# Optimization experiments

Measured on AMD Instinct MI355X. Metric: run time of the kernel, lower is better.

Reference implementation:

```python
import jax, jax.numpy as jnp
import numpy as np

B, CIN, COUT, T, H, W, NH = 8, 16, 16, 32, 16, 16, 4
DIN = CIN * H * W    # 4096
DOUT = COUT * H * W  # 4096
DH = DOUT // NH      # 1024


def conv3d(x, w, b, pad):
    y = jax.lax.conv_general_dilated(
        x, w, window_strides=(1, 1, 1), padding=((pad, pad),) * 3,
        dimension_numbers=('NCDHW', 'OIDHW', 'NCDHW'))
    return y + b[None, :, None, None, None]


def instance_norm(x, eps=1e-5):
    # InstanceNorm3d default: no affine, normalize per (B,C) over (T,H,W)
    mu = x.mean(axis=(2, 3, 4), keepdims=True)
    var = ((x - mu) ** 2).mean(axis=(2, 3, 4), keepdims=True)
    return (x - mu) * jax.lax.rsqrt(var + eps)


def slstm(x, Wg, bg, Rg):
    # x: (B,T,D). Wg: (4,D,D) input weights [i,f,z,o]; bg: (4,D);
    # Rg: (NH,4,DH,DH) block-diagonal per-head recurrent weights.
    Bb, Tt, D = x.shape
    Gx = jnp.einsum('btd,god->btgo', x, Wg) + bg  # (B,T,4,D)

    def step(carry, gx):
        h, c, n, m = carry
        hh = h.reshape(Bb, NH, DH)
        gh = jnp.einsum('bhd,hgod->bhgo', hh, Rg)          # (B,NH,4,DH)
        pre = gx + gh.transpose(0, 2, 1, 3).reshape(Bb, 4, D)
        i_pre, f_pre, z_pre, o_pre = pre[:, 0], pre[:, 1], pre[:, 2], pre[:, 3]
        # stabilized exponential gating (xLSTM sLSTM)
        m_new = jnp.maximum(f_pre + m, i_pre)
        i = jnp.exp(i_pre - m_new)
        f = jnp.exp(f_pre + m - m_new)
        c = f * c + i * jnp.tanh(z_pre)
        n = f * n + i
        h = jax.nn.sigmoid(o_pre) * c / n
        return (h, c, n, m_new), h

    init = tuple(jnp.zeros((Bb, D), x.dtype) for _ in range(4))
    _, hs = jax.lax.scan(step, init, Gx.transpose(1, 0, 2, 3))  # hs: (T,B,D)
    return hs.transpose(1, 0, 2)


def setup_inputs():
    key = jax.random.key(0)
    ks = jax.random.split(key, 8)
    s = 0.02
    return {
        'x': jax.random.normal(ks[0], (B, CIN, T, H, W), jnp.float32),
        'c1_w': jax.random.normal(ks[1], (COUT, CIN, 3, 3, 3), jnp.float32) * 0.05,
        'c1_b': jnp.zeros((COUT,), jnp.float32),
        'c2_w': jax.random.normal(ks[2], (COUT, COUT, 3, 3, 3), jnp.float32) * 0.05,
        'c2_b': jnp.zeros((COUT,), jnp.float32),
        'c3_w': jax.random.normal(ks[3], (COUT, COUT, 3, 3, 3), jnp.float32) * 0.05,
        'c3_b': jnp.zeros((COUT,), jnp.float32),
        'pre_w': jax.random.normal(ks[4], (DOUT, DIN), jnp.float32) * s,
        'pre_b': jnp.zeros((DOUT,), jnp.float32),
        'lstm_W': jax.random.normal(ks[5], (4, DOUT, DOUT), jnp.float32) * s,
        'lstm_b': jnp.zeros((4, DOUT), jnp.float32),
        'lstm_R': jax.random.normal(ks[6], (NH, 4, DH, DH), jnp.float32) * s,
        'attn_w': jax.random.normal(ks[7], (1, 2 * COUT), jnp.float32) * 0.05,
        'attn_b': jnp.zeros((1,), jnp.float32),
    }


def reference(x, c1_w, c1_b, c2_w, c2_b, c3_w, c3_b, pre_w, pre_b,
              lstm_W, lstm_b, lstm_R, attn_w, attn_b):
    # conv3d branch: conv -> IN -> relu -> conv -> relu -> conv -> relu
    y = jax.nn.relu(instance_norm(conv3d(x, c1_w, c1_b, 1)))
    y = jax.nn.relu(conv3d(y, c2_w, c2_b, 1))
    out3d = jax.nn.relu(conv3d(y, c3_w, c3_b, 1))
    # sLSTM branch
    xs = x.transpose(0, 2, 1, 3, 4).reshape(B, T, DIN)
    xs = xs @ pre_w.T + pre_b
    hs = slstm(xs, lstm_W, lstm_b, lstm_R)                 # (B,T,DOUT)
    s_out = hs.reshape(B, T, COUT, H, W).transpose(0, 2, 1, 3, 4)
    # attention-gated fusion: cat -> 1x1x1 conv -> sigmoid -> weighted sum
    comb = jnp.concatenate([s_out, out3d], axis=1)         # (B,2*COUT,T,H,W)
    alpha = jax.nn.sigmoid(jnp.einsum('bcthw,oc->bothw', comb, attn_w)
                           + attn_b[None, :, None, None, None])
    return alpha * out3d + (1 - alpha) * s_out
```

## Files before the change

kernel.cpp:

```cpp
#include <hip/hip_runtime.h>
#include <hip/hip_bf16.h>
#include <cstddef>

#define BB   8
#define CIN  16
#define COUT 16
#define TT   32
#define HH   16
#define WW   16
#define DIN  4096
#define DOUT 4096
#define NH   4
#define DH   1024
#define SPAT 8192
#define NSEQ 256

typedef __attribute__((ext_vector_type(8))) short  bf16x8;
typedef __attribute__((ext_vector_type(4))) float  f32x4;
typedef __attribute__((ext_vector_type(4))) unsigned short us4;
typedef __attribute__((ext_vector_type(4))) int    i32x4;
typedef unsigned short ushort_t;
typedef unsigned long long u64_t;

static __device__ __forceinline__ ushort_t f2bf(float f) {
    union { float f; unsigned u; } v; v.f = f;
    unsigned r = (v.u + 0x7fffu + ((v.u >> 16) & 1u)) >> 16;
    return (ushort_t)r;
}
static __device__ __forceinline__ float bf2f(ushort_t u) {
    union { unsigned u; float f; } v; v.u = ((unsigned)u) << 16;
    return v.f;
}

__global__ void setup_kernel(const float* __restrict__ x, ushort_t* __restrict__ xt,
                             const float* __restrict__ w1, const float* __restrict__ w2,
                             const float* __restrict__ w3,
                             float* __restrict__ cw1, float* __restrict__ cw2,
                             float* __restrict__ cw3, int* __restrict__ flags) {
    int bid = blockIdx.x;
    if (bid < 1024) {
        int idx = bid * 256 + threadIdx.x;
        int n = idx >> 10, k4 = (idx & 1023) * 4;
        int b = n >> 5, t = n & 31, c = k4 >> 8, hw = k4 & 255;
        f32x4 f = *(const f32x4*)&x[(((size_t)(b * CIN + c) * TT + t)) * 256 + hw];
        us4 o;
        #pragma unroll
        for (int i = 0; i < 4; ++i) o[i] = f2bf(f[i]);
        *(us4*)&xt[(size_t)n * DIN + k4] = o;
    } else if (bid < 1105) {
        int i = (bid - 1024) * 256 + threadIdx.x;
        if (i < 3 * 6912) {
            int set = i / 6912, j = i - set * 6912;
            const float* w = (set == 0) ? w1 : (set == 1) ? w2 : w3;
            float* cw      = (set == 0) ? cw1 : (set == 1) ? cw2 : cw3;
            int o = j & 15, r = j >> 4;
            int k = r % 27, ci = r / 27;
            cw[j] = w[(size_t)(o * CIN + ci) * 27 + k];
        }
    } else {
        int j = (bid - 1105) * 256 + threadIdx.x;
        if (j < 2176)
            ((i32x4*)flags)[j] = (i32x4){0, 0, 0, 0};
    }
}

template<int BN, int BK, bool OUT_BF16, bool ADD_BIAS>
__device__ __forceinline__
void gemm_body(char* smem, int bx, int by, int nsplit,
               const ushort_t* __restrict__ A, const float* __restrict__ B,
               const float* __restrict__ bias, void* __restrict__ C,
               int N, int K) {
    constexpr int NF  = BN / 16;
    constexpr int TPR = 256 / BN;
    constexpr int FPT = BK / TPR;
    ushort_t* Al = (ushort_t*)smem;
    ushort_t* Bl = Al + 2 * 256 * BK;
    int tid  = threadIdx.x;
    int lane = tid & 63;
    int wv   = tid >> 6;
    int n0 = bx * BN;
    int ksp = K / nsplit;
    int kS  = by * ksp;

    f32x4 acc[4][NF];
    #pragma unroll
    for (int i = 0; i < 4; ++i)
        #pragma unroll
        for (int j = 0; j < NF; ++j) acc[i][j] = (f32x4){0.f, 0.f, 0.f, 0.f};

    auto stageA = [&](int buf, int k0) {
        #pragma unroll
        for (int q = 0; q < 8; ++q) {
            int rbase = wv * 64 + q * 8;
            int row = rbase + (lane >> 3);
            const ushort_t* g = A + (size_t)row * K + k0 + (lane & 7) * 8;
            __builtin_amdgcn_global_load_lds(
                (const __attribute__((address_space(1))) void*)g,
                (__attribute__((address_space(3))) void*)&Al[(buf * 256 + rbase) * BK],
                16, 0, 0);
        }
    };
    auto stageB = [&](int buf, int k0) {
        int r  = tid / TPR;
        int cs = (tid % TPR) * FPT;
        const float* g = B + (size_t)(n0 + r) * K + k0 + cs;
        #pragma unroll
        for (int q = 0; q < FPT / 4; ++q) {
            f32x4 f = *(const f32x4*)(g + q * 4);
            us4 pk;
            #pragma unroll
            for (int e = 0; e < 4; ++e) pk[e] = f2bf(f[e]);
            *(us4*)&Bl[(buf * BN + r) * BK + cs + q * 4] = pk;
        }
    };
    auto compute = [&](int buf) {
        #pragma unroll
        for (int ks = 0; ks < BK / 32; ++ks) {
            bf16x8 af[4], bfr[NF];
            #pragma unroll
            for (int i = 0; i < 4; ++i)
                af[i] = *(const bf16x8*)&Al[(buf * 256 + wv * 64 + i * 16 + (lane & 15)) * BK + ks * 32 + (lane >> 4) * 8];
            #pragma unroll
            for (int j = 0; j < NF; ++j)
                bfr[j] = *(const bf16x8*)&Bl[(buf * BN + j * 16 + (lane & 15)) * BK + ks * 32 + (lane >> 4) * 8];
            #pragma unroll
            for (int i = 0; i < 4; ++i)
                #pragma unroll
                for (int j = 0; j < NF; ++j)
                    acc[i][j] = __builtin_amdgcn_mfma_f32_16x16x32_bf16(af[i], bfr[j], acc[i][j], 0, 0, 0);
        }
    };

    stageA(0, kS); stageB(0, kS);
    __syncthreads();
    int nk = ksp / BK;
    int cur = 0;
    for (int t = 0; t < nk; ++t) {
        if (t + 1 < nk) { stageA(cur ^ 1, kS + (t + 1) * BK); stageB(cur ^ 1, kS + (t + 1) * BK); }
        compute(cur);
        __syncthreads();
        cur ^= 1;
    }

    size_t cofs = (size_t)by * 256 * N;
    #pragma unroll
    for (int i = 0; i < 4; ++i) {
        int row = wv * 64 + i * 16 + (lane >> 4) * 4;
        #pragma unroll
        for (int j = 0; j < NF; ++j) {
            int col = n0 + j * 16 + (lane & 15);
            float bv = ADD_BIAS ? bias[col] : 0.f;
            #pragma unroll
            for (int r = 0; r < 4; ++r) {
                float v = acc[i][j][r] + bv;
                if constexpr (OUT_BF16) ((ushort_t*)C)[cofs + (size_t)(row + r) * N + col] = f2bf(v);
                else                    ((float*)C)[cofs + (size_t)(row + r) * N + col] = v;
            }
        }
    }
}

__device__ __forceinline__
void conv_taps(const float* xin, const float* __restrict__ cw, int half,
               const float* __restrict__ bias, float* accs, int tid) {
    int h = tid >> 4, wx = tid & 15;
    f32x4 a0 = *(const f32x4*)&bias[half * 8];
    f32x4 a1 = *(const f32x4*)&bias[half * 8 + 4];
    for (int ci = 0; ci < CIN; ++ci) {
        #pragma unroll
        for (int kt = 0; kt < 3; ++kt) {
            #pragma unroll
            for (int kh = 0; kh < 3; ++kh) {
                int h2 = h + kh - 1;
                bool vh = (unsigned)h2 < HH;
                int h2c = vh ? h2 : 0;
                #pragma unroll
                for (int kw = 0; kw < 3; ++kw) {
                    int w2 = wx + kw - 1;
                    bool v = vh && ((unsigned)w2 < WW);
                    int w2c = ((unsigned)w2 < WW) ? w2 : 0;
                    float xv = xin[(ci * 3 + kt) * 256 + h2c * 16 + w2c];
                    xv = v ? xv : 0.f;
                    const float* wp = cw + (size_t)(ci * 27 + kt * 9 + kh * 3 + kw) * 16 + half * 8;
                    f32x4 w0 = *(const f32x4*)(wp);
                    f32x4 w1 = *(const f32x4*)(wp + 4);
                    a0 += xv * w0; a1 += xv * w1;
                }
            }
        }
    }
    #pragma unroll
    for (int i = 0; i < 4; ++i) { accs[i] = a0[i]; accs[4 + i] = a1[i]; }
}

__device__ __forceinline__
void conv1_body(char* smem, int blk,
                const float* __restrict__ in, const float* __restrict__ cw,
                const float* __restrict__ bias,
                float* __restrict__ out, float* __restrict__ psum) {
    float* xin = (float*)smem;
    int b = blk >> 6, t = (blk >> 1) & 31, half = blk & 1;
    int tid = threadIdx.x;

    for (int i = tid; i < CIN * 3 * 256; i += 256) {
        int hw = i & 255, r = i >> 8;
        int kt = r % 3, ci = r / 3;
        int tt = t + kt - 1;
        float v = 0.f;
        if ((unsigned)tt < TT)
            v = in[((size_t)(b * CIN + ci) * TT + tt) * 256 + hw];
        xin[(ci * 3 + kt) * 256 + hw] = v;
    }
    __syncthreads();

    float accs[8];
    conv_taps(xin, cw, half, bias, accs, tid);
    #pragma unroll
    for (int o = 0; o < 8; ++o)
        out[((size_t)(b * COUT + half * 8 + o) * TT + t) * 256 + tid] = accs[o];

    __syncthreads();
    float* sm = xin;
    int wv = tid >> 6;
    #pragma unroll
    for (int o = 0; o < 8; ++o) {
        float s = accs[o];
        float q = accs[o] * accs[o];
        #pragma unroll
        for (int m = 1; m < 64; m <<= 1) {
            s += __shfl_xor(s, m, 64);
            q += __shfl_xor(q, m, 64);
        }
        if ((tid & 63) == 0) { sm[wv * 16 + o * 2] = s; sm[wv * 16 + o * 2 + 1] = q; }
    }
    __syncthreads();
    if (tid < 16) {
        int o = tid >> 1, which = tid & 1;
        float v = sm[o * 2 + which] + sm[16 + o * 2 + which]
                + sm[32 + o * 2 + which] + sm[48 + o * 2 + which];
        psum[((((size_t)(b * 32 + t) * 2 + half) * 8 + o) * 2) + which] = v;
    }
}

__device__ __forceinline__
void conv2_body(char* smem, int blk,
                const float* __restrict__ y1, const float* __restrict__ cw,
                const float* __restrict__ bias, const float* __restrict__ psum,
                float* __restrict__ y2, int* __restrict__ cflags) {
    float* xin = (float*)smem;
    float* sstats = xin + 12288;
    int b = blk >> 6, t = (blk >> 1) & 31, half = blk & 1;
    int tid = threadIdx.x;

    if (tid < 16) {
        int c = tid;
        float sum = 0.f, sq = 0.f;
        for (int t2 = 0; t2 < 32; ++t2) {
            size_t base = (((size_t)(b * 32 + t2) * 2 + (c >> 3)) * 8 + (c & 7)) * 2;
            sum += psum[base];
            sq  += psum[base + 1];
        }
        float mu = sum / (float)SPAT;
        float var = sq / (float)SPAT - mu * mu;
        sstats[c * 2]     = mu;
        sstats[c * 2 + 1] = rsqrtf(var + 1e-5f);
    }
    __syncthreads();

    for (int i = tid; i < CIN * 3 * 256; i += 256) {
        int hw = i & 255, r = i >> 8;
        int kt = r % 3, ci = r / 3;
        int tt = t + kt - 1;
        float v = 0.f;
        if ((unsigned)tt < TT) {
            v = y1[((size_t)(b * CIN + ci) * TT + tt) * 256 + hw];
            v = fmaxf((v - sstats[ci * 2]) * sstats[ci * 2 + 1], 0.f);
        }
        xin[(ci * 3 + kt) * 256 + hw] = v;
    }
    __syncthreads();

    float accs[8];
    conv_taps(xin, cw, half, bias, accs, tid);
    #pragma unroll
    for (int o = 0; o < 8; ++o) {
        float v = fmaxf(accs[o], 0.f);
        __hip_atomic_store(&y2[((size_t)(b * COUT + half * 8 + o) * TT + t) * 256 + tid],
                           v, __ATOMIC_RELAXED, __HIP_MEMORY_SCOPE_AGENT);
    }
    __syncthreads();
    if (tid == 0)
        __hip_atomic_store(&cflags[blk], 1, __ATOMIC_RELAXED, __HIP_MEMORY_SCOPE_AGENT);
}

__device__ __forceinline__
void conv3_body(char* smem, int blk,
                const float* __restrict__ y2, const float* __restrict__ cw,
                const float* __restrict__ bias, float* __restrict__ out3d,
                const int* __restrict__ cflags) {
    float* xin = (float*)smem;
    int b = blk >> 6, t = (blk >> 1) & 31, half = blk & 1;
    int tid = threadIdx.x;

    if (tid == 0) {
        #pragma unroll
        for (int dt = -1; dt <= 1; ++dt) {
            int tn = t + dt;
            if ((unsigned)tn >= TT) continue;
            #pragma unroll
            for (int hh = 0; hh < 2; ++hh) {
                const int* f = &cflags[(b << 6) | (tn << 1) | hh];
                while (__hip_atomic_load(f, __ATOMIC_RELAXED,
                                         __HIP_MEMORY_SCOPE_AGENT) == 0)
                    __builtin_amdgcn_s_sleep(1);
            }
        }
    }
    __syncthreads();

    for (int i = tid; i < CIN * 3 * 256; i += 256) {
        int hw = i & 255, r = i >> 8;
        int kt = r % 3, ci = r / 3;
        int tt = t + kt - 1;
        float v = 0.f;
        if ((unsigned)tt < TT)
            v = __hip_atomic_load(&y2[((size_t)(b * CIN + ci) * TT + tt) * 256 + hw],
                                  __ATOMIC_RELAXED, __HIP_MEMORY_SCOPE_AGENT);
        xin[(ci * 3 + kt) * 256 + hw] = v;
    }
    __syncthreads();

    float accs[8];
    conv_taps(xin, cw, half, bias, accs, tid);
    #pragma unroll
    for (int o = 0; o < 8; ++o)
        out3d[((size_t)(b * COUT + half * 8 + o) * TT + t) * 256 + tid] = fmaxf(accs[o], 0.f);
}

__global__ __launch_bounds__(256, 2)
void fused1_kernel(const ushort_t* __restrict__ xt, const float* __restrict__ pre_w,
                   const float* __restrict__ pre_b, ushort_t* __restrict__ xs2b,
                   const float* __restrict__ x, const float* __restrict__ cw1,
                   const float* __restrict__ c1_b, float* __restrict__ y1,
                   float* __restrict__ psum) {
    extern __shared__ char smem[];
    if (blockIdx.x < 256)
        gemm_body<16, 64, true, true>(smem, blockIdx.x, 0, 1, xt, pre_w, pre_b, xs2b, DOUT, DIN);
    else
        conv1_body(smem, blockIdx.x - 256, x, cw1, c1_b, y1, psum);
}

__global__ __launch_bounds__(256, 2)
void fused2_kernel(const ushort_t* __restrict__ xs2b, const float* __restrict__ lstm_W,
                   float* __restrict__ Gx,
                   const float* __restrict__ y1, const float* __restrict__ cw2,
                   const float* __restrict__ c2_b, const float* __restrict__ psum,
                   float* __restrict__ y2,
                   const float* __restrict__ cw3, const float* __restrict__ c3_b,
                   float* __restrict__ out3d, int* __restrict__ cflags) {
    extern __shared__ char smem[];
    if (blockIdx.x < 1024)
        gemm_body<32, 64, false, false>(smem, blockIdx.x & 511, blockIdx.x >> 9, 2,
                                        xs2b, lstm_W, nullptr, Gx, 4 * DOUT, DOUT);
    else if (blockIdx.x < 1536)
        conv2_body(smem, blockIdx.x - 1024, y1, cw2, c2_b, psum, y2, cflags);
    else
        conv3_body(smem, blockIdx.x - 1536, y2, cw3, c3_b, out3d, cflags);
}

#define GXPS ((size_t)NSEQ * 4 * DOUT)

__global__ __launch_bounds__(256, 1)
void lstm_persist_kernel(const float* __restrict__ R,
                         const float* __restrict__ Gx,
                         const float* __restrict__ lstm_b,
                         unsigned* __restrict__ hfr,
                         int* __restrict__ flags,
                         const float* __restrict__ out3d,
                         const float* __restrict__ attn_w,
                         const float* __restrict__ attn_b,
                         float* __restrict__ out) {
    __shared__ ushort_t Rl[4][32][64 * 8];
    __shared__ float gh_p[4][4][16][8];

    int tid  = threadIdx.x;
    int lane = tid & 63;
    int w    = tid >> 6;
    int head = blockIdx.x >> 6;
    int oc   = blockIdx.x & 63;

    #pragma unroll 4
    for (int n = 0; n < 64; ++n) {
        int g = n >> 4, r = n & 15;
        const float* src = R + ((size_t)((head * 4 + g) * DH + oc * 16 + r)) * DH + tid * 4;
        f32x4 f = *(const f32x4*)src;
        int k0 = tid * 4;
        int ks = k0 >> 5;
        int kI = (k0 >> 3) & 3;
        int e8 = k0 & 7;
        union { ushort_t u[4]; u64_t q; } pk;
        #pragma unroll
        for (int e = 0; e < 4; ++e) pk.u[e] = f2bf(f[e]);
        *(u64_t*)&Rl[g][ks][((kI << 4) | r) * 8 + e8] = pk.q;
    }

    int arow = lane & 15;
    int part = arow >> 3;
    int bb   = arow & 7;
    int kseg = lane >> 4;

    int gb  = tid >> 4;
    int gol = tid & 15;
    int gd  = head * DH + oc * 16 + gol;
    int o_h = oc * 16 + gol;
    unsigned hslot = ((unsigned)head * 32 + (o_h >> 5)) * 256 + gb * 32 + (o_h & 31);
    float c_r = 0.f, n_r = 0.f, m_r = 0.f;
    float lb0 = 0.f, lb1 = 0.f, lb2 = 0.f, lb3 = 0.f;
    if (tid < 128) {
        lb0 = lstm_b[gd];
        lb1 = lstm_b[DOUT + gd];
        lb2 = lstm_b[2 * DOUT + gd];
        lb3 = lstm_b[3 * DOUT + gd];
    }

    __syncthreads();

    for (int t = 0; t < TT; ++t) {
        float gx0 = lb0, gx1 = lb1, gx2 = lb2, gx3 = lb3;
        if (tid < 128) {
            size_t gxoff = ((size_t)(gb * TT + t)) * (4 * DOUT) + gd;
            #pragma unroll
            for (int p = 0; p < 2; ++p) {
                const float* gp = Gx + p * GXPS + gxoff;
                gx0 += gp[0];
                gx1 += gp[DOUT];
                gx2 += gp[2 * DOUT];
                gx3 += gp[3 * DOUT];
            }
        }

        if (t > 0) {
            const int* fl = flags + (((t - 1) * 4 + head) << 6);
            for (;;) {
                int v = __hip_atomic_load(fl + lane, __ATOMIC_RELAXED,
                                          __HIP_MEMORY_SCOPE_AGENT);
                if (__all(v != 0)) break;
                __builtin_amdgcn_s_sleep(1);
            }

            const u64_t* hb = (const u64_t*)hfr
                + ((((size_t)(t - 1) * 4 + head) * 32) * 256 + bb * 32 + kseg * 8) / 2;
            bf16x8 hf[8];
            #pragma unroll
            for (int j = 0; j < 8; ++j) {
                const u64_t* p = hb + (size_t)(w * 8 + j) * 128;
                union { ushort_t u[8]; bf16x8 v; } fr;
                #pragma unroll
                for (int e2 = 0; e2 < 4; ++e2) {
                    u64_t q = __hip_atomic_load(p + e2, __ATOMIC_RELAXED,
                                                __HIP_MEMORY_SCOPE_AGENT);
                    unsigned q0 = (unsigned)q, q1 = (unsigned)(q >> 32);
                    fr.u[e2 * 2]     = part ? (ushort_t)(q0 >> 16) : (ushort_t)(q0 & 0xffffu);
                    fr.u[e2 * 2 + 1] = part ? (ushort_t)(q1 >> 16) : (ushort_t)(q1 & 0xffffu);
                }
                hf[j] = fr.v;
            }

            f32x4 acc[4];
            #pragma unroll
            for (int g = 0; g < 4; ++g) acc[g] = (f32x4){0.f, 0.f, 0.f, 0.f};
            #pragma unroll
            for (int g = 0; g < 4; ++g)
                #pragma unroll
                for (int j = 0; j < 8; ++j) {
                    bf16x8 a = *(const bf16x8*)&Rl[g][w * 8 + j][lane * 8];
                    acc[g] = __builtin_amdgcn_mfma_f32_16x16x32_bf16(a, hf[j], acc[g], 0, 0, 0);
                }
            #pragma unroll
            for (int g = 0; g < 4; ++g)
                #pragma unroll
                for (int r = 0; r < 4; ++r)
                    acc[g][r] += __shfl_xor(acc[g][r], 8, 64);
            if (part == 0) {
                int orow0 = kseg * 4;
                #pragma unroll
                for (int g = 0; g < 4; ++g)
                    #pragma unroll
                    for (int r = 0; r < 4; ++r)
                        gh_p[w][g][orow0 + r][bb] = acc[g][r];
            }
        } else {
            for (int i = tid; i < 4 * 4 * 16 * 8; i += 256)
                ((float*)gh_p)[i] = 0.f;
        }
        __syncthreads();

        if (tid < 128) {
            float ip = gx0 +
                gh_p[0][0][gol][gb] + gh_p[1][0][gol][gb] + gh_p[2][0][gol][gb] + gh_p[3][0][gol][gb];
            float fp = gx1 +
                gh_p[0][1][gol][gb] + gh_p[1][1][gol][gb] + gh_p[2][1][gol][gb] + gh_p[3][1][gol][gb];
            float zp = gx2 +
                gh_p[0][2][gol][gb] + gh_p[1][2][gol][gb] + gh_p[2][2][gol][gb] + gh_p[3][2][gol][gb];
            float op = gx3 +
                gh_p[0][3][gol][gb] + gh_p[1][3][gol][gb] + gh_p[2][3][gol][gb] + gh_p[3][3][gol][gb];
            float mn = fmaxf(fp + m_r, ip);
            float iv = __expf(ip - mn);
            float fv = __expf(fp + m_r - mn);
            float zc = fminf(fmaxf(zp, -9.f), 9.f);
            float th = 1.f - 2.f / (__expf(2.f * zc) + 1.f);
            c_r = fv * c_r + iv * th;
            n_r = fv * n_r + iv;
            float sig = 1.f / (1.f + __expf(-op));
            float hv = sig * c_r / n_r;
            m_r = mn;
            unsigned hi = f2bf(hv);
            unsigned lo = f2bf(hv - bf2f((ushort_t)hi));
            __hip_atomic_store(&hfr[(size_t)t * 32768 + hslot],
                               hi | (lo << 16),
                               __ATOMIC_RELAXED, __HIP_MEMORY_SCOPE_AGENT);
        }
        __syncthreads();
        if (tid == 0)
            __hip_atomic_store(&flags[((t * 4 + head) << 6) + oc], 1,
                               __ATOMIC_RELAXED, __HIP_MEMORY_SCOPE_AGENT);
    }

    {
        const int* fl31 = flags + ((31 * 4) << 6);
        for (;;) {
            int ok = 1;
            #pragma unroll
            for (int q = 0; q < 4; ++q)
                ok &= (__hip_atomic_load(fl31 + q * 64 + lane, __ATOMIC_RELAXED,
                                         __HIP_MEMORY_SCOPE_AGENT) != 0);
            if (__all(ok)) break;
            __builtin_amdgcn_s_sleep(1);
        }

        int idx = blockIdx.x * 256 + tid;
        int hw = idx & 255;
        int tC = (idx >> 8) & 31;
        int bC = idx >> 13;
        float dot = attn_b[0];
        float sv[16], ov[16];
        #pragma unroll
        for (int ch = 0; ch < 16; ++ch) {
            int d = ch * 256 + hw;
            int hd2 = d >> 10, o_h2 = d & 1023;
            size_t slot = (size_t)tC * 32768 + (size_t)hd2 * 8192
                        + (o_h2 >> 5) * 256 + bC * 32 + (o_h2 & 31);
            unsigned v32 = __hip_atomic_load(&hfr[slot], __ATOMIC_RELAXED,
                                             __HIP_MEMORY_SCOPE_AGENT);
            float s = bf2f((ushort_t)(v32 & 0xffffu)) + bf2f((ushort_t)(v32 >> 16));
            float o3 = out3d[(((size_t)(bC * COUT + ch) * TT + tC)) * 256 + hw];
            sv[ch] = s; ov[ch] = o3;
            dot += attn_w[ch] * s + attn_w[16 + ch] * o3;
        }
        float alpha = 1.f / (1.f + expf(-dot));
        #pragma unroll
        for (int ch = 0; ch < 16; ++ch) {
            out[(((size_t)(bC * COUT + ch) * TT + tC)) * 256 + hw] =
                alpha * ov[ch] + (1.f - alpha) * sv[ch];
        }
    }
}

extern "C" void kernel_launch(void* const* d_in, const int* in_sizes, int n_in,
                              void* d_out, int out_size, void* d_ws, size_t ws_size,
                              hipStream_t stream) {
    const float* x      = (const float*)d_in[0];
    const float* c1_w   = (const float*)d_in[1];
    const float* c1_b   = (const float*)d_in[2];
    const float* c2_w   = (const float*)d_in[3];
    const float* c2_b   = (const float*)d_in[4];
    const float* c3_w   = (const float*)d_in[5];
    const float* c3_b   = (const float*)d_in[6];
    const float* pre_w  = (const float*)d_in[7];
    const float* pre_b  = (const float*)d_in[8];
    const float* lstm_W = (const float*)d_in[9];
    const float* lstm_b = (const float*)d_in[10];
    const float* lstm_R = (const float*)d_in[11];
    const float* attn_w = (const float*)d_in[12];
    const float* attn_b = (const float*)d_in[13];
    float* out = (float*)d_out;

    float* wsf = (float*)d_ws;
    float* y1    = wsf;
    float* y2    = y1 + 1048576;
    float* out3d = y2 + 1048576;
    float* Gx    = out3d + 1048576;
    float* cw1   = Gx + 2 * 4194304;
    float* cw2   = cw1 + 6912;
    float* cw3   = cw2 + 6912;
    float* psum  = cw3 + 6912;
    float* pad   = psum + 8192;
    ushort_t* xt   = (ushort_t*)(pad + 64);
    ushort_t* xs2b = xt + 1048576;
    unsigned* hfr  = (unsigned*)(xs2b + 1048576);
    int*     flags = (int*)(hfr + 1048576);
    int*    cflags = flags + 8192;

    setup_kernel<<<1114, 256, 0, stream>>>(x, xt, c1_w, c2_w, c3_w, cw1, cw2, cw3, flags);

    fused1_kernel<<<768, 256, 69632, stream>>>(xt, pre_w, pre_b, xs2b,
                                               x, cw1, c1_b, y1, psum);

    fused2_kernel<<<2048, 256, 73728, stream>>>(xs2b, lstm_W, Gx,
                                                y1, cw2, c2_b, psum, y2,
                                                cw3, c3_b, out3d, cflags);

    lstm_persist_kernel<<<256, 256, 0, stream>>>(lstm_R, Gx, lstm_b, hfr, flags,
                                                 out3d, attn_w, attn_b, out);
}
```

Baseline: 528.6 us.

## Move input-gate GEMM into persistent LSTM kernel prologue, drop split-K

Moves the Gx = xs @ W GEMM out of the fused conv kernel and into a prologue of the persistent sLSTM kernel. Each of the 256 blocks computes the gate preactivations for exactly the 16 columns per gate that it consumes in the recurrence, adds the bias, and writes them to a block-private buffer. This removes the split-K partial sums, the double Gx read in the recurrence, and the contention between GEMM and conv work in fused2. The cost is that the GEMM now runs on only 256 blocks at one block per CU, serialized before the recurrence, and the conv kernel no longer overlaps with it.

```diff
diff --git a/kernel.cpp b/kernel.cpp
--- a/kernel.cpp
+++ b/kernel.cpp
@@ -66,7 +66,7 @@
 
 template<int BN, int BK, bool OUT_BF16, bool ADD_BIAS>
 __device__ __forceinline__
-void gemm_body(char* smem, int bx, int by, int nsplit,
+void gemm_body(char* smem, int bx,
                const ushort_t* __restrict__ A, const float* __restrict__ B,
                const float* __restrict__ bias, void* __restrict__ C,
                int N, int K) {
@@ -79,8 +79,6 @@
     int lane = tid & 63;
     int wv   = tid >> 6;
     int n0 = bx * BN;
-    int ksp = K / nsplit;
-    int kS  = by * ksp;
 
     f32x4 acc[4][NF];
     #pragma unroll
@@ -131,18 +129,17 @@
         }
     };
 
-    stageA(0, kS); stageB(0, kS);
-    __syncthreads();
-    int nk = ksp / BK;
+    stageA(0, 0); stageB(0, 0);
+    __syncthreads();
+    int nk = K / BK;
     int cur = 0;
     for (int t = 0; t < nk; ++t) {
-        if (t + 1 < nk) { stageA(cur ^ 1, kS + (t + 1) * BK); stageB(cur ^ 1, kS + (t + 1) * BK); }
+        if (t + 1 < nk) { stageA(cur ^ 1, (t + 1) * BK); stageB(cur ^ 1, (t + 1) * BK); }
         compute(cur);
         __syncthreads();
         cur ^= 1;
     }
 
-    size_t cofs = (size_t)by * 256 * N;
     #pragma unroll
     for (int i = 0; i < 4; ++i) {
         int row = wv * 64 + i * 16 + (lane >> 4) * 4;
@@ -153,8 +150,8 @@
             #pragma unroll
             for (int r = 0; r < 4; ++r) {
                 float v = acc[i][j][r] + bv;
-                if constexpr (OUT_BF16) ((ushort_t*)C)[cofs + (size_t)(row + r) * N + col] = f2bf(v);
-                else                    ((float*)C)[cofs + (size_t)(row + r) * N + col] = v;
+                if constexpr (OUT_BF16) ((ushort_t*)C)[(size_t)(row + r) * N + col] = f2bf(v);
+                else                    ((float*)C)[(size_t)(row + r) * N + col] = v;
             }
         }
     }
@@ -345,50 +342,127 @@
                    float* __restrict__ psum) {
     extern __shared__ char smem[];
     if (blockIdx.x < 256)
-        gemm_body<16, 64, true, true>(smem, blockIdx.x, 0, 1, xt, pre_w, pre_b, xs2b, DOUT, DIN);
+        gemm_body<16, 64, true, true>(smem, blockIdx.x, xt, pre_w, pre_b, xs2b, DOUT, DIN);
     else
         conv1_body(smem, blockIdx.x - 256, x, cw1, c1_b, y1, psum);
 }
 
 __global__ __launch_bounds__(256, 2)
-void fused2_kernel(const ushort_t* __restrict__ xs2b, const float* __restrict__ lstm_W,
-                   float* __restrict__ Gx,
-                   const float* __restrict__ y1, const float* __restrict__ cw2,
+void fused2_kernel(const float* __restrict__ y1, const float* __restrict__ cw2,
                    const float* __restrict__ c2_b, const float* __restrict__ psum,
                    float* __restrict__ y2,
                    const float* __restrict__ cw3, const float* __restrict__ c3_b,
                    float* __restrict__ out3d, int* __restrict__ cflags) {
     extern __shared__ char smem[];
-    if (blockIdx.x < 1024)
-        gemm_body<32, 64, false, false>(smem, blockIdx.x & 511, blockIdx.x >> 9, 2,
-                                        xs2b, lstm_W, nullptr, Gx, 4 * DOUT, DOUT);
-    else if (blockIdx.x < 1536)
-        conv2_body(smem, blockIdx.x - 1024, y1, cw2, c2_b, psum, y2, cflags);
+    if (blockIdx.x < 512)
+        conv2_body(smem, blockIdx.x, y1, cw2, c2_b, psum, y2, cflags);
     else
-        conv3_body(smem, blockIdx.x - 1536, y2, cw3, c3_b, out3d, cflags);
-}
-
-#define GXPS ((size_t)NSEQ * 4 * DOUT)
+        conv3_body(smem, blockIdx.x - 512, y2, cw3, c3_b, out3d, cflags);
+}
 
 __global__ __launch_bounds__(256, 1)
 void lstm_persist_kernel(const float* __restrict__ R,
-                         const float* __restrict__ Gx,
+                         const ushort_t* __restrict__ xs2b,
+                         const float* __restrict__ lstm_W,
                          const float* __restrict__ lstm_b,
+                         float* __restrict__ Gxp,
                          unsigned* __restrict__ hfr,
                          int* __restrict__ flags,
                          const float* __restrict__ out3d,
                          const float* __restrict__ attn_w,
                          const float* __restrict__ attn_b,
                          float* __restrict__ out) {
-    __shared__ ushort_t Rl[4][32][64 * 8];
-    __shared__ float gh_p[4][4][16][8];
+    __shared__ char smem[139264];
 
     int tid  = threadIdx.x;
     int lane = tid & 63;
     int w    = tid >> 6;
     int head = blockIdx.x >> 6;
     int oc   = blockIdx.x & 63;
-
+    int gcbase = head * DH + oc * 16;
+
+    {
+        ushort_t* Al = (ushort_t*)smem;
+        ushort_t* Bl = Al + 2 * 256 * 64;
+        f32x4 acc[4][4];
+        #pragma unroll
+        for (int i = 0; i < 4; ++i)
+            #pragma unroll
+            for (int j = 0; j < 4; ++j) acc[i][j] = (f32x4){0.f, 0.f, 0.f, 0.f};
+
+        auto stageA = [&](int buf, int k0) {
+            #pragma unroll
+            for (int q = 0; q < 8; ++q) {
+                int rbase = w * 64 + q * 8;
+                int row = rbase + (lane >> 3);
+                const ushort_t* g = xs2b + (size_t)row * DIN + k0 + (lane & 7) * 8;
+                __builtin_amdgcn_global_load_lds(
+                    (const __attribute__((address_space(1))) void*)g,
+                    (__attribute__((address_space(3))) void*)&Al[(buf * 256 + rbase) * 64],
+                    16, 0, 0);
+            }
+        };
+        auto stageB = [&](int buf, int k0) {
+            int r = tid >> 2;
+            int g = r >> 4, ol = r & 15;
+            size_t gc = (size_t)g * DOUT + gcbase + ol;
+            int cs = (tid & 3) * 16;
+            const float* p = lstm_W + gc * DOUT + k0 + cs;
+            #pragma unroll
+            for (int q = 0; q < 4; ++q) {
+                f32x4 f = *(const f32x4*)(p + q * 4);
+                us4 pk;
+                #pragma unroll
+                for (int e = 0; e < 4; ++e) pk[e] = f2bf(f[e]);
+                *(us4*)&Bl[(buf * 64 + r) * 64 + cs + q * 4] = pk;
+            }
+        };
+        auto compute = [&](int buf) {
+            #pragma unroll
+            for (int ks = 0; ks < 2; ++ks) {
+                bf16x8 af[4], bfr[4];
+                #pragma unroll
+                for (int i = 0; i < 4; ++i)
+                    af[i] = *(const bf16x8*)&Al[(buf * 256 + w * 64 + i * 16 + (lane & 15)) * 64 + ks * 32 + (lane >> 4) * 8];
+                #pragma unroll
+                for (int j = 0; j < 4; ++j)
+                    bfr[j] = *(const bf16x8*)&Bl[(buf * 64 + j * 16 + (lane & 15)) * 64 + ks * 32 + (lane >> 4) * 8];
+                #pragma unroll
+                for (int i = 0; i < 4; ++i)
+                    #pragma unroll
+                    for (int j = 0; j < 4; ++j)
+                        acc[i][j] = __builtin_amdgcn_mfma_f32_16x16x32_bf16(af[i], bfr[j], acc[i][j], 0, 0, 0);
+            }
+        };
+
+        stageA(0, 0); stageB(0, 0);
+        __syncthreads();
+        int cur = 0;
+        for (int t = 0; t < 64; ++t) {
+            if (t + 1 < 64) { stageA(cur ^ 1, (t + 1) * 64); stageB(cur ^ 1, (t + 1) * 64); }
+            compute(cur);
+            __syncthreads();
+            cur ^= 1;
+        }
+
+        float* myGx = Gxp + (size_t)blockIdx.x * 16384;
+        #pragma unroll
+        for (int i = 0; i < 4; ++i) {
+            int row = w * 64 + i * 16 + (lane >> 4) * 4;
+            #pragma unroll
+            for (int j = 0; j < 4; ++j) {
+                int ol = lane & 15;
+                float bv = lstm_b[(size_t)j * DOUT + gcbase + ol];
+                #pragma unroll
+                for (int r = 0; r < 4; ++r)
+                    myGx[((j * 256 + row + r) << 4) + ol] = acc[i][j][r] + bv;
+            }
+        }
+    }
+    __syncthreads();
+
+    ushort_t* Rl = (ushort_t*)smem;
+    float* gh_p  = (float*)(smem + 131072);
     #pragma unroll 4
     for (int n = 0; n < 64; ++n) {
         int g = n >> 4, r = n & 15;
@@ -401,7 +475,7 @@
         union { ushort_t u[4]; u64_t q; } pk;
         #pragma unroll
         for (int e = 0; e < 4; ++e) pk.u[e] = f2bf(f[e]);
-        *(u64_t*)&Rl[g][ks][((kI << 4) | r) * 8 + e8] = pk.q;
+        *(u64_t*)&Rl[((g * 32 + ks) << 9) + ((kI << 4) | r) * 8 + e8] = pk.q;
     }
 
     int arow = lane & 15;
@@ -411,32 +485,21 @@
 
     int gb  = tid >> 4;
     int gol = tid & 15;
-    int gd  = head * DH + oc * 16 + gol;
     int o_h = oc * 16 + gol;
     unsigned hslot = ((unsigned)head * 32 + (o_h >> 5)) * 256 + gb * 32 + (o_h & 31);
     float c_r = 0.f, n_r = 0.f, m_r = 0.f;
-    float lb0 = 0.f, lb1 = 0.f, lb2 = 0.f, lb3 = 0.f;
-    if (tid < 128) {
-        lb0 = lstm_b[gd];
-        lb1 = lstm_b[DOUT + gd];
-        lb2 = lstm_b[2 * DOUT + gd];
-        lb3 = lstm_b[3 * DOUT + gd];
-    }
+    const float* myGx = Gxp + (size_t)blockIdx.x * 16384;
 
     __syncthreads();
 
     for (int t = 0; t < TT; ++t) {
-        float gx0 = lb0, gx1 = lb1, gx2 = lb2, gx3 = lb3;
+        float gx0 = 0.f, gx1 = 0.f, gx2 = 0.f, gx3 = 0.f;
         if (tid < 128) {
-            size_t gxoff = ((size_t)(gb * TT + t)) * (4 * DOUT) + gd;
-            #pragma unroll
-            for (int p = 0; p < 2; ++p) {
-                const float* gp = Gx + p * GXPS + gxoff;
-                gx0 += gp[0];
-                gx1 += gp[DOUT];
-                gx2 += gp[2 * DOUT];
-                gx3 += gp[3 * DOUT];
-            }
+            const float* gp = myGx + (((gb * 32 + t)) << 4) + gol;
+            gx0 = gp[0];
+            gx1 = gp[1 * 4096];
+            gx2 = gp[2 * 4096];
+            gx3 = gp[3 * 4096];
         }
 
         if (t > 0) {
@@ -473,7 +536,7 @@
             for (int g = 0; g < 4; ++g)
                 #pragma unroll
                 for (int j = 0; j < 8; ++j) {
-                    bf16x8 a = *(const bf16x8*)&Rl[g][w * 8 + j][lane * 8];
+                    bf16x8 a = *(const bf16x8*)&Rl[((g * 32 + w * 8 + j) << 9) + lane * 8];
                     acc[g] = __builtin_amdgcn_mfma_f32_16x16x32_bf16(a, hf[j], acc[g], 0, 0, 0);
                 }
             #pragma unroll
@@ -487,23 +550,27 @@
                 for (int g = 0; g < 4; ++g)
                     #pragma unroll
                     for (int r = 0; r < 4; ++r)
-                        gh_p[w][g][orow0 + r][bb] = acc[g][r];
+                        gh_p[(((w * 4 + g) * 16 + orow0 + r) << 3) + bb] = acc[g][r];
             }
         } else {
             for (int i = tid; i < 4 * 4 * 16 * 8; i += 256)
-                ((float*)gh_p)[i] = 0.f;
+                gh_p[i] = 0.f;
         }
         __syncthreads();
 
         if (tid < 128) {
             float ip = gx0 +
-                gh_p[0][0][gol][gb] + gh_p[1][0][gol][gb] + gh_p[2][0][gol][gb] + gh_p[3][0][gol][gb];
+                gh_p[(((0 * 4 + 0) * 16 + gol) << 3) + gb] + gh_p[(((1 * 4 + 0) * 16 + gol) << 3) + gb] +
+                gh_p[(((2 * 4 + 0) * 16 + gol) << 3) + gb] + gh_p[(((3 * 4 + 0) * 16 + gol) << 3) + gb];
             float fp = gx1 +
-                gh_p[0][1][gol][gb] + gh_p[1][1][gol][gb] + gh_p[2][1][gol][gb] + gh_p[3][1][gol][gb];
+                gh_p[(((0 * 4 + 1) * 16 + gol) << 3) + gb] + gh_p[(((1 * 4 + 1) * 16 + gol) << 3) + gb] +
+                gh_p[(((2 * 4 + 1) * 16 + gol) << 3) + gb] + gh_p[(((3 * 4 + 1) * 16 + gol) << 3) + gb];
             float zp = gx2 +
-                gh_p[0][2][gol][gb] + gh_p[1][2][gol][gb] + gh_p[2][2][gol][gb] + gh_p[3][2][gol][gb];
+                gh_p[(((0 * 4 + 2) * 16 + gol) << 3) + gb] + gh_p[(((1 * 4 + 2) * 16 + gol) << 3) + gb] +
+                gh_p[(((2 * 4 + 2) * 16 + gol) << 3) + gb] + gh_p[(((3 * 4 + 2) * 16 + gol) << 3) + gb];
             float op = gx3 +
-                gh_p[0][3][gol][gb] + gh_p[1][3][gol][gb] + gh_p[2][3][gol][gb] + gh_p[3][3][gol][gb];
+                gh_p[(((0 * 4 + 3) * 16 + gol) << 3) + gb] + gh_p[(((1 * 4 + 3) * 16 + gol) << 3) + gb] +
+                gh_p[(((2 * 4 + 3) * 16 + gol) << 3) + gb] + gh_p[(((3 * 4 + 3) * 16 + gol) << 3) + gb];
             float mn = fmaxf(fp + m_r, ip);
             float iv = __expf(ip - mn);
             float fv = __expf(fp + m_r - mn);
@@ -589,8 +656,8 @@
     float* y1    = wsf;
     float* y2    = y1 + 1048576;
     float* out3d = y2 + 1048576;
-    float* Gx    = out3d + 1048576;
-    float* cw1   = Gx + 2 * 4194304;
+    float* Gxp   = out3d + 1048576;
+    float* cw1   = Gxp + 4194304;
     float* cw2   = cw1 + 6912;
     float* cw3   = cw2 + 6912;
     float* psum  = cw3 + 6912;
@@ -606,10 +673,10 @@
     fused1_kernel<<<768, 256, 69632, stream>>>(xt, pre_w, pre_b, xs2b,
                                                x, cw1, c1_b, y1, psum);
 
-    fused2_kernel<<<2048, 256, 73728, stream>>>(xs2b, lstm_W, Gx,
-                                                y1, cw2, c2_b, psum, y2,
+    fused2_kernel<<<1024, 256, 49408, stream>>>(y1, cw2, c2_b, psum, y2,
                                                 cw3, c3_b, out3d, cflags);
 
-    lstm_persist_kernel<<<256, 256, 0, stream>>>(lstm_R, Gx, lstm_b, hfr, flags,
+    lstm_persist_kernel<<<256, 256, 0, stream>>>(lstm_R, xs2b, lstm_W, lstm_b,
+                                                 Gxp, hfr, flags,
                                                  out3d, attn_w, attn_b, out);
 }
```

New measurement: 535.6 us. Within noise of the previous version (+1.3%).

## Widen GEMM N-tiles, drop split-K and fold LSTM bias into Gx GEMM

Applied to the files above, without the earlier changes.

Both projection GEMMs now use 64-wide N tiles, which cuts the block counts from 256 to 64 for the first and from 1024 to 256 for the second. The second GEMM no longer splits K in two, so it writes a single Gx buffer with the LSTM bias already added. The persistent LSTM kernel then loads one Gx value per gate instead of two partials plus bias. In exchange, each GEMM block does more serial K work and far fewer GEMM blocks run alongside the conv blocks, which may leave the GPU less fully loaded. In return, fewer re-reads of the A operand are needed and the Gx write and read traffic is halved.

```diff
diff --git a/kernel.cpp b/kernel.cpp
--- a/kernel.cpp
+++ b/kernel.cpp
@@ -64,9 +64,9 @@
     }
 }
 
-template<int BN, int BK, bool OUT_BF16, bool ADD_BIAS>
+template<int BN, int BK, bool OUT_BF16>
 __device__ __forceinline__
-void gemm_body(char* smem, int bx, int by, int nsplit,
+void gemm_body(char* smem, int bx,
                const ushort_t* __restrict__ A, const float* __restrict__ B,
                const float* __restrict__ bias, void* __restrict__ C,
                int N, int K) {
@@ -79,8 +79,6 @@
     int lane = tid & 63;
     int wv   = tid >> 6;
     int n0 = bx * BN;
-    int ksp = K / nsplit;
-    int kS  = by * ksp;
 
     f32x4 acc[4][NF];
     #pragma unroll
@@ -131,30 +129,29 @@
         }
     };
 
-    stageA(0, kS); stageB(0, kS);
-    __syncthreads();
-    int nk = ksp / BK;
+    stageA(0, 0); stageB(0, 0);
+    __syncthreads();
+    int nk = K / BK;
     int cur = 0;
     for (int t = 0; t < nk; ++t) {
-        if (t + 1 < nk) { stageA(cur ^ 1, kS + (t + 1) * BK); stageB(cur ^ 1, kS + (t + 1) * BK); }
+        if (t + 1 < nk) { stageA(cur ^ 1, (t + 1) * BK); stageB(cur ^ 1, (t + 1) * BK); }
         compute(cur);
         __syncthreads();
         cur ^= 1;
     }
 
-    size_t cofs = (size_t)by * 256 * N;
     #pragma unroll
     for (int i = 0; i < 4; ++i) {
         int row = wv * 64 + i * 16 + (lane >> 4) * 4;
         #pragma unroll
         for (int j = 0; j < NF; ++j) {
             int col = n0 + j * 16 + (lane & 15);
-            float bv = ADD_BIAS ? bias[col] : 0.f;
+            float bv = bias[col];
             #pragma unroll
             for (int r = 0; r < 4; ++r) {
                 float v = acc[i][j][r] + bv;
-                if constexpr (OUT_BF16) ((ushort_t*)C)[cofs + (size_t)(row + r) * N + col] = f2bf(v);
-                else                    ((float*)C)[cofs + (size_t)(row + r) * N + col] = v;
+                if constexpr (OUT_BF16) ((ushort_t*)C)[(size_t)(row + r) * N + col] = f2bf(v);
+                else                    ((float*)C)[(size_t)(row + r) * N + col] = v;
             }
         }
     }
@@ -344,36 +341,32 @@
                    const float* __restrict__ c1_b, float* __restrict__ y1,
                    float* __restrict__ psum) {
     extern __shared__ char smem[];
-    if (blockIdx.x < 256)
-        gemm_body<16, 64, true, true>(smem, blockIdx.x, 0, 1, xt, pre_w, pre_b, xs2b, DOUT, DIN);
+    if (blockIdx.x < 64)
+        gemm_body<64, 64, true>(smem, blockIdx.x, xt, pre_w, pre_b, xs2b, DOUT, DIN);
     else
-        conv1_body(smem, blockIdx.x - 256, x, cw1, c1_b, y1, psum);
+        conv1_body(smem, blockIdx.x - 64, x, cw1, c1_b, y1, psum);
 }
 
 __global__ __launch_bounds__(256, 2)
 void fused2_kernel(const ushort_t* __restrict__ xs2b, const float* __restrict__ lstm_W,
-                   float* __restrict__ Gx,
+                   const float* __restrict__ lstm_b, float* __restrict__ Gx,
                    const float* __restrict__ y1, const float* __restrict__ cw2,
                    const float* __restrict__ c2_b, const float* __restrict__ psum,
                    float* __restrict__ y2,
                    const float* __restrict__ cw3, const float* __restrict__ c3_b,
                    float* __restrict__ out3d, int* __restrict__ cflags) {
     extern __shared__ char smem[];
-    if (blockIdx.x < 1024)
-        gemm_body<32, 64, false, false>(smem, blockIdx.x & 511, blockIdx.x >> 9, 2,
-                                        xs2b, lstm_W, nullptr, Gx, 4 * DOUT, DOUT);
-    else if (blockIdx.x < 1536)
-        conv2_body(smem, blockIdx.x - 1024, y1, cw2, c2_b, psum, y2, cflags);
+    if (blockIdx.x < 256)
+        gemm_body<64, 64, false>(smem, blockIdx.x, xs2b, lstm_W, lstm_b, Gx, 4 * DOUT, DOUT);
+    else if (blockIdx.x < 768)
+        conv2_body(smem, blockIdx.x - 256, y1, cw2, c2_b, psum, y2, cflags);
     else
-        conv3_body(smem, blockIdx.x - 1536, y2, cw3, c3_b, out3d, cflags);
-}
-
-#define GXPS ((size_t)NSEQ * 4 * DOUT)
+        conv3_body(smem, blockIdx.x - 768, y2, cw3, c3_b, out3d, cflags);
+}
 
 __global__ __launch_bounds__(256, 1)
 void lstm_persist_kernel(const float* __restrict__ R,
                          const float* __restrict__ Gx,
-                         const float* __restrict__ lstm_b,
                          unsigned* __restrict__ hfr,
                          int* __restrict__ flags,
                          const float* __restrict__ out3d,
@@ -415,28 +408,17 @@
     int o_h = oc * 16 + gol;
     unsigned hslot = ((unsigned)head * 32 + (o_h >> 5)) * 256 + gb * 32 + (o_h & 31);
     float c_r = 0.f, n_r = 0.f, m_r = 0.f;
-    float lb0 = 0.f, lb1 = 0.f, lb2 = 0.f, lb3 = 0.f;
-    if (tid < 128) {
-        lb0 = lstm_b[gd];
-        lb1 = lstm_b[DOUT + gd];
-        lb2 = lstm_b[2 * DOUT + gd];
-        lb3 = lstm_b[3 * DOUT + gd];
-    }
 
     __syncthreads();
 
     for (int t = 0; t < TT; ++t) {
-        float gx0 = lb0, gx1 = lb1, gx2 = lb2, gx3 = lb3;
+        float gx0 = 0.f, gx1 = 0.f, gx2 = 0.f, gx3 = 0.f;
         if (tid < 128) {
             size_t gxoff = ((size_t)(gb * TT + t)) * (4 * DOUT) + gd;
-            #pragma unroll
-            for (int p = 0; p < 2; ++p) {
-                const float* gp = Gx + p * GXPS + gxoff;
-                gx0 += gp[0];
-                gx1 += gp[DOUT];
-                gx2 += gp[2 * DOUT];
-                gx3 += gp[3 * DOUT];
-            }
+            gx0 = Gx[gxoff];
+            gx1 = Gx[gxoff + DOUT];
+            gx2 = Gx[gxoff + 2 * DOUT];
+            gx3 = Gx[gxoff + 3 * DOUT];
         }
 
         if (t > 0) {
@@ -590,7 +572,7 @@
     float* y2    = y1 + 1048576;
     float* out3d = y2 + 1048576;
     float* Gx    = out3d + 1048576;
-    float* cw1   = Gx + 2 * 4194304;
+    float* cw1   = Gx + 4194304;
     float* cw2   = cw1 + 6912;
     float* cw3   = cw2 + 6912;
     float* psum  = cw3 + 6912;
@@ -603,13 +585,13 @@
 
     setup_kernel<<<1114, 256, 0, stream>>>(x, xt, c1_w, c2_w, c3_w, cw1, cw2, cw3, flags);
 
-    fused1_kernel<<<768, 256, 69632, stream>>>(xt, pre_w, pre_b, xs2b,
+    fused1_kernel<<<576, 256, 81920, stream>>>(xt, pre_w, pre_b, xs2b,
                                                x, cw1, c1_b, y1, psum);
 
-    fused2_kernel<<<2048, 256, 73728, stream>>>(xs2b, lstm_W, Gx,
+    fused2_kernel<<<1280, 256, 81920, stream>>>(xs2b, lstm_W, lstm_b, Gx,
                                                 y1, cw2, c2_b, psum, y2,
                                                 cw3, c3_b, out3d, cflags);
 
-    lstm_persist_kernel<<<256, 256, 0, stream>>>(lstm_R, Gx, lstm_b, hfr, flags,
+    lstm_persist_kernel<<<256, 256, 0, stream>>>(lstm_R, Gx, hfr, flags,
                                                  out3d, attn_w, attn_b, out);
 }
```

Measured after the change: 526.6 us (median of 2 runs). About the same (-0.4%).
